# Optimization experiments

Measured on AMD Instinct MI355X. Metric: run time of the kernel, lower is better.

## Reference

```python
import jax, jax.numpy as jnp
import numpy as np

B, SV, SQ, D = 32, 4096, 1152, 128
FD = 96  # feature_dim (adaptive pool target and batchnorm channels)
BN_EPS = 1e-5


def setup_inputs() -> dict:
    key = jax.random.key(0)
    k1, k2, k3, k4 = jax.random.split(key, 4)
    return {
        'q': jax.random.normal(k1, (B, SQ, D), dtype=jnp.float32),
        'v': jax.random.normal(k2, (B, SV, D), dtype=jnp.float32),
        'h_mat': jax.random.normal(k3, (1, 3, FD, 1), dtype=jnp.float32),
        'h_bias': jax.random.normal(k4, (1, 3, 1, 1), dtype=jnp.float32),
        'gamma': jnp.ones((FD,), dtype=jnp.float32),
        'beta': jnp.zeros((FD,), dtype=jnp.float32),
    }


def reference(q, v, h_mat, h_bias, gamma, beta):
    b, sv, d = v.shape
    sq = q.shape[1]
    # einsum 'bijk,hcxk,bqiv->bjck' with a=[B,1,Sv,D], h_mat=[1,3,FD,1], b=[B,1,D,Sq]
    # (k broadcasts 1->D, i broadcasts 1->D) factorizes into independent sums:
    sumq = jnp.sum(q, axis=(1, 2))                 # [B] = sum_{i,v} b[b,0,i,v]
    hm = jnp.sum(h_mat, axis=(0, 2, 3))            # [3] = sum_{h,x} h_mat
    # att_maps (post transpose(1,2)): [B,3,Sv,D]
    att = (v[:, None, :, :] * hm[None, :, None, None] * sumq[:, None, None, None]
           + h_bias.reshape(1, 3, 1, 1))
    att = att / jnp.linalg.norm(att, axis=2, keepdims=True)  # L2 norm over Sv
    att = jax.nn.softmax(att, axis=2)                        # softmax over Sv

    # logits = einsum('bikj,bhi,bqvk->bivq', a1, att[:,:,0,:], b1)  -> [B,D,Sq,1]
    att0sum = att[:, :, 0, :].sum(axis=1)          # [B,D] sum over h of att_maps[:,:,0,:]
    qr = q.reshape(b, d, sq)                        # faithful to torch .view memory reshape
    vs = v.sum(axis=1)                              # [B,D] = sum_j a1[b,0,k,j]
    inner = jnp.einsum('bkv,bk->bv', qr, vs)        # [B,Sq]
    logits0 = att0sum[:, :, None] * inner[:, None, :]  # [B,D,Sq]
    # AdaptiveAvgPool1d(FD) on last dim (Sq multiple of FD -> reshape+mean), then transpose
    logits = logits0.reshape(b, d, FD, sq // FD).mean(axis=-1).transpose(0, 2, 1)  # [B,FD,D]

    # loop i=1..h_-1: einsum('bihc,bxv,bqkv->bi') -> per-batch scalar, pooled to [B,FD,1]
    vsum = v.sum(axis=(1, 2))                       # [B]
    qs = qr.sum(axis=2)                             # [B,D] = sum_k b1[b,0,k,v]
    for i in (1, 2):
        attisum = att[:, :, i, :].sum(axis=1)       # [B,D]
        li = vsum * jnp.sum(attisum * qs, axis=1)   # [B]
        logits = logits + li[:, None, None]         # broadcast add of [B,1,1]

    # BatchNorm1d(FD) in training mode: stats over (batch, length) per channel
    mean = logits.mean(axis=(0, 2), keepdims=True)
    var = logits.var(axis=(0, 2), keepdims=True)
    out = (logits - mean) * jax.lax.rsqrt(var + BN_EPS)
    out = out * gamma[None, :, None] + beta[None, :, None]
    return out
```

## Files before the change

kernel.cpp:

```cpp
#include <hip/hip_runtime.h>
#include <math.h>

#define BB 32
#define SV 4096
#define SQ 1152
#define DD 128
#define FD 96
#define NS 32
#define RPC (SV / NS)
#define LOG2E 1.44269504088896340f

#define OFF_G    0
#define OFF_P    393216
#define OFF_ATT0 1179648
#define OFF_LI   1183744
#define OFF_A0   1183776
#define OFF_A0S  1183808
#define OFF_IP   1183840
#define OFF_BNA  1186912
#define OFF_BNB  1187008

__global__ __launch_bounds__(256) void k_pass1(const float* __restrict__ q,
                                               const float* __restrict__ v,
                                               float* __restrict__ ws) {
    __shared__ float red[6][8][DD];
    if (blockIdx.x < 1024) {
        int b = blockIdx.x >> 5, chunk = blockIdx.x & 31;
        int lane = threadIdx.x & 31, rowg = threadIdx.x >> 5;
        int d0 = lane * 4;
        const float* base = v + ((size_t)b * SV + (size_t)chunk * RPC) * DD;
        float s1[4] = {}, s2[4] = {}, s3[4] = {}, s4[4] = {}, s5[4] = {}, s6[4] = {};
        for (int i = 0; i < RPC / 8; i++) {
            float4 x = *reinterpret_cast<const float4*>(base + (size_t)(rowg + 8 * i) * DD + d0);
            float vv[4] = {x.x, x.y, x.z, x.w};
#pragma unroll
            for (int j = 0; j < 4; j++) {
                float a = vv[j], a2 = a * a, a4 = a2 * a2;
                s1[j] += a;       s2[j] += a2;      s3[j] += a2 * a;
                s4[j] += a4;      s5[j] += a4 * a;  s6[j] += a4 * a2;
            }
        }
#pragma unroll
        for (int j = 0; j < 4; j++) {
            red[0][rowg][d0 + j] = s1[j]; red[1][rowg][d0 + j] = s2[j];
            red[2][rowg][d0 + j] = s3[j]; red[3][rowg][d0 + j] = s4[j];
            red[4][rowg][d0 + j] = s5[j]; red[5][rowg][d0 + j] = s6[j];
        }
        __syncthreads();
        for (int t = threadIdx.x; t < 6 * DD; t += 256) {
            int m = t >> 7, d = t & (DD - 1);
            float a = 0;
#pragma unroll
            for (int r = 0; r < 8; r++) a += red[m][r][d];
            ws[OFF_P + ((size_t)(b * NS + chunk) * 6 + m) * DD + d] = a;
        }
    } else {
        int g = (blockIdx.x - 1024) * 256 + threadIdx.x;
        const float4* p = reinterpret_cast<const float4*>(q + (size_t)g * 12);
        float4 a = p[0], b4 = p[1], c = p[2];
        ws[OFF_G + g] = ((a.x + a.y) + (a.z + a.w)) + ((b4.x + b4.y) + (b4.z + b4.w))
                      + ((c.x + c.y) + (c.z + c.w));
    }
}

__global__ __launch_bounds__(256) void k_finalize(const float* __restrict__ v,
                                                  const float* __restrict__ hmat,
                                                  const float* __restrict__ hbias,
                                                  float* __restrict__ ws) {
    int b = blockIdx.x, tid = threadIdx.x;
    __shared__ float Gl[DD * 97];
    __shared__ float qsl[DD], svl[DD];
    __shared__ float hm_l[3], hb_l[3];
    __shared__ float redc[10];
    __shared__ float sumq_sh;
    const float* Gb = ws + OFF_G + (size_t)b * DD * FD;
#pragma unroll
    for (int i = 0; i < 12; i++) {
        int idx = (i * 256 + tid) * 4;
        float4 x = *reinterpret_cast<const float4*>(Gb + idx);
        float xv[4] = {x.x, x.y, x.z, x.w};
#pragma unroll
        for (int j = 0; j < 4; j++) {
            int e = idx + j, dd = e / 96, f = e - dd * 96;
            Gl[dd * 97 + f] = xv[j];
        }
    }
    if (tid >= 128 && tid < 131) {
        int c = tid - 128;
        float h = 0;
        for (int x2 = 0; x2 < FD; x2++) h += hmat[c * FD + x2];
        hm_l[c] = h; hb_l[c] = hbias[c];
    }
    __syncthreads();
    float M1 = 0, M2 = 0, M3 = 0, M4 = 0, M5 = 0, M6 = 0;
    if (tid < 128) {
        const float* P = ws + OFF_P;
#pragma unroll 4
        for (int ch = 0; ch < NS; ch++) {
            const float* p = P + (size_t)(b * NS + ch) * 6 * DD + tid;
            M1 += p[0];      M2 += p[DD];     M3 += p[2 * DD];
            M4 += p[3 * DD]; M5 += p[4 * DD]; M6 += p[5 * DD];
        }
        svl[tid] = M1;
    } else {
        int d = tid - 128;
        float qs = 0;
#pragma unroll 8
        for (int f = 0; f < FD; f++) qs += Gl[d * 97 + f];
        qsl[d] = qs;
    }
    __syncthreads();
    if (tid < 64) {
        float x = qsl[tid] + qsl[tid + 64];
#pragma unroll
        for (int ofs = 32; ofs; ofs >>= 1) x += __shfl_xor(x, ofs, 64);
        if (tid == 0) sumq_sh = x;
    }
    __syncthreads();
    if (tid < 128) {
        float sumq = sumq_sh;
        float v0 = v[((size_t)b * SV + 0) * DD + tid];
        float v1 = v[((size_t)b * SV + 1) * DD + tid];
        float v2 = v[((size_t)b * SV + 2) * DD + tid];
        float att0 = 0, att1 = 0, att2 = 0;
#pragma unroll
        for (int c = 0; c < 3; c++) {
            float alpha = hm_l[c] * sumq, hb = hb_l[c];
            float n2 = alpha * alpha * M2 + 2.f * alpha * hb * M1 + (float)SV * hb * hb;
            float tt = alpha / sqrtf(n2);
            float Z = (float)SV + tt * (M1 + tt * (0.5f * M2 + tt * ((1.f / 6.f) * M3
                    + tt * ((1.f / 24.f) * M4 + tt * ((1.f / 120.f) * M5
                    + tt * (1.f / 720.f) * M6)))));
            float rz = 1.f / Z, tl = tt * LOG2E;
            att0 += exp2f(v0 * tl) * rz;
            att1 += exp2f(v1 * tl) * rz;
            att2 += exp2f(v2 * tl) * rz;
        }
        ws[OFF_ATT0 + b * DD + tid] = att0;
        float qsv = qsl[tid];
        float vals[5] = {att0, att0 * att0, att1 * qsv, att2 * qsv, M1};
#pragma unroll
        for (int i = 0; i < 5; i++) {
            float x = vals[i];
#pragma unroll
            for (int ofs = 32; ofs; ofs >>= 1) x += __shfl_xor(x, ofs, 64);
            if ((tid & 63) == 0) redc[(tid >> 6) * 5 + i] = x;
        }
    }
    __syncthreads();
    if (tid == 0) {
        float a0 = redc[0] + redc[5], a0s = redc[1] + redc[6];
        float r1 = redc[2] + redc[7], r2 = redc[3] + redc[8], vs = redc[4] + redc[9];
        ws[OFF_A0 + b] = a0; ws[OFF_A0S + b] = a0s;
        ws[OFF_LI + b] = vs * (r1 + r2);
    }
    if (tid < FD) {
        float ip = 0;
#pragma unroll 8
        for (int k = 0; k < DD; k++) ip += svl[k] * Gl[k * 97 + tid];
        ws[OFF_IP + b * FD + tid] = ip * (1.0f / 12.0f);
    }
}

__global__ void k_bnstats(const float* __restrict__ gamma, const float* __restrict__ beta,
                          float* __restrict__ ws) {
    const float* ipb = ws + OFF_IP; const float* A0b = ws + OFF_A0;
    const float* A0sb = ws + OFF_A0S; const float* lib = ws + OFF_LI;
    float* bnA = ws + OFF_BNA; float* bnB = ws + OFF_BNB;
    int f = threadIdx.x;
    if (f >= FD) return;
    double Sm = 0, Se2 = 0, Sl = 0;
#pragma unroll 4
    for (int b = 0; b < BB; b++) {
        double ip = ipb[b * FD + f], a0 = A0b[b], a0s = A0sb[b], l = lib[b];
        Sm += ip * a0;
        Se2 += ip * ip * a0s + 2.0 * ip * l * a0 + (double)DD * l * l;
        Sl += l;
    }
    double mean = Sm / ((double)BB * DD) + Sl / (double)BB;
    double var = Se2 / ((double)BB * DD) - mean * mean;
    double rstd = 1.0 / sqrt(var + 1e-5);
    float A = (float)rstd * gamma[f];
    bnA[f] = A; bnB[f] = beta[f] - (float)mean * A;
}

__global__ void k_out(const float* __restrict__ ws, float* __restrict__ out) {
    const float* att0b = ws + OFF_ATT0; const float* ipb = ws + OFF_IP;
    const float* lib = ws + OFF_LI;
    const float* bnA = ws + OFF_BNA; const float* bnB = ws + OFF_BNB;
    int idx = blockIdx.x * blockDim.x + threadIdx.x;
    int k = idx & (DD - 1);
    int bf = idx >> 7;
    int f = bf % FD;
    int b = bf / FD;
    out[idx] = (att0b[b * DD + k] * ipb[b * FD + f] + lib[b]) * bnA[f] + bnB[f];
}

extern "C" void kernel_launch(void* const* d_in, const int* in_sizes, int n_in,
                              void* d_out, int out_size, void* d_ws, size_t ws_size,
                              hipStream_t stream) {
    const float* q     = (const float*)d_in[0];
    const float* v     = (const float*)d_in[1];
    const float* hmat  = (const float*)d_in[2];
    const float* hbias = (const float*)d_in[3];
    const float* gamma = (const float*)d_in[4];
    const float* beta  = (const float*)d_in[5];
    float* out = (float*)d_out;
    float* ws = (float*)d_ws;

    k_pass1<<<2560, 256, 0, stream>>>(q, v, ws);
    k_finalize<<<BB, 256, 0, stream>>>(v, hmat, hbias, ws);
    k_bnstats<<<1, 128, 0, stream>>>(gamma, beta, ws);
    k_out<<<(BB * FD * DD) / 256, 256, 0, stream>>>(ws, out);
}
```

Measured before the change: 126.1 us.

## Fuse BN stats into output kernel, widen finalize, and cut v-reduction chunks

```diff
diff --git a/kernel.cpp b/kernel.cpp
--- a/kernel.cpp
+++ b/kernel.cpp
@@ -6,26 +6,24 @@
 #define SQ 1152
 #define DD 128
 #define FD 96
-#define NS 32
+#define NS 8
 #define RPC (SV / NS)
 #define LOG2E 1.44269504088896340f
 
 #define OFF_G    0
 #define OFF_P    393216
-#define OFF_ATT0 1179648
-#define OFF_LI   1183744
-#define OFF_A0   1183776
-#define OFF_A0S  1183808
-#define OFF_IP   1183840
-#define OFF_BNA  1186912
-#define OFF_BNB  1187008
+#define OFF_ATT0 589824
+#define OFF_LI   593920
+#define OFF_A0   593952
+#define OFF_A0S  593984
+#define OFF_IP   594016
 
 __global__ __launch_bounds__(256) void k_pass1(const float* __restrict__ q,
                                                const float* __restrict__ v,
                                                float* __restrict__ ws) {
     __shared__ float red[6][8][DD];
-    if (blockIdx.x < 1024) {
-        int b = blockIdx.x >> 5, chunk = blockIdx.x & 31;
+    if (blockIdx.x < 256) {
+        int b = blockIdx.x >> 3, chunk = blockIdx.x & 7;
         int lane = threadIdx.x & 31, rowg = threadIdx.x >> 5;
         int d0 = lane * 4;
         const float* base = v + ((size_t)b * SV + (size_t)chunk * RPC) * DD;
@@ -55,7 +53,7 @@
             ws[OFF_P + ((size_t)(b * NS + chunk) * 6 + m) * DD + d] = a;
         }
     } else {
-        int g = (blockIdx.x - 1024) * 256 + threadIdx.x;
+        int g = (blockIdx.x - 256) * 256 + threadIdx.x;
         const float4* p = reinterpret_cast<const float4*>(q + (size_t)g * 12);
         float4 a = p[0], b4 = p[1], c = p[2];
         ws[OFF_G + g] = ((a.x + a.y) + (a.z + a.w)) + ((b4.x + b4.y) + (b4.z + b4.w))
@@ -63,20 +61,28 @@
     }
 }
 
-__global__ __launch_bounds__(256) void k_finalize(const float* __restrict__ v,
-                                                  const float* __restrict__ hmat,
-                                                  const float* __restrict__ hbias,
-                                                  float* __restrict__ ws) {
+__global__ __launch_bounds__(1024) void k_finalize(const float* __restrict__ v,
+                                                   const float* __restrict__ hmat,
+                                                   const float* __restrict__ hbias,
+                                                   float* __restrict__ ws) {
     int b = blockIdx.x, tid = threadIdx.x;
     __shared__ float Gl[DD * 97];
-    __shared__ float qsl[DD], svl[DD];
+    __shared__ float Ml[6][DD];
+    __shared__ float qsl[DD];
+    __shared__ float pp[8][FD];
     __shared__ float hm_l[3], hb_l[3];
     __shared__ float redc[10];
     __shared__ float sumq_sh;
+    float v0 = 0, v1 = 0, v2 = 0;
+    if (tid < DD) {
+        v0 = v[((size_t)b * SV + 0) * DD + tid];
+        v1 = v[((size_t)b * SV + 1) * DD + tid];
+        v2 = v[((size_t)b * SV + 2) * DD + tid];
+    }
     const float* Gb = ws + OFF_G + (size_t)b * DD * FD;
 #pragma unroll
-    for (int i = 0; i < 12; i++) {
-        int idx = (i * 256 + tid) * 4;
+    for (int i = 0; i < 3; i++) {
+        int idx = (i * 1024 + tid) * 4;
         float4 x = *reinterpret_cast<const float4*>(Gb + idx);
         float xv[4] = {x.x, x.y, x.z, x.w};
 #pragma unroll
@@ -85,29 +91,29 @@
             Gl[dd * 97 + f] = xv[j];
         }
     }
-    if (tid >= 128 && tid < 131) {
-        int c = tid - 128;
-        float h = 0;
-        for (int x2 = 0; x2 < FD; x2++) h += hmat[c * FD + x2];
-        hm_l[c] = h; hb_l[c] = hbias[c];
-    }
-    __syncthreads();
-    float M1 = 0, M2 = 0, M3 = 0, M4 = 0, M5 = 0, M6 = 0;
-    if (tid < 128) {
-        const float* P = ws + OFF_P;
-#pragma unroll 4
-        for (int ch = 0; ch < NS; ch++) {
-            const float* p = P + (size_t)(b * NS + ch) * 6 * DD + tid;
-            M1 += p[0];      M2 += p[DD];     M3 += p[2 * DD];
-            M4 += p[3 * DD]; M5 += p[4 * DD]; M6 += p[5 * DD];
-        }
-        svl[tid] = M1;
-    } else {
-        int d = tid - 128;
-        float qs = 0;
-#pragma unroll 8
-        for (int f = 0; f < FD; f++) qs += Gl[d * 97 + f];
-        qsl[d] = qs;
+    if (tid < 6 * DD) {
+        int m = tid >> 7, d = tid & (DD - 1);
+        const float* p = ws + OFF_P + (size_t)b * NS * 6 * DD + m * DD + d;
+        float a = 0;
+#pragma unroll
+        for (int ch = 0; ch < NS; ch++) a += p[(size_t)ch * 6 * DD];
+        Ml[m][d] = a;
+    } else if (tid >= 768 && tid < 864) {
+        int t2 = tid - 768, c = t2 >> 5, x = t2 & 31;
+        float h = hmat[c * FD + x] + hmat[c * FD + x + 32] + hmat[c * FD + x + 64];
+        h += __shfl_xor(h, 1, 64); h += __shfl_xor(h, 2, 64);
+        h += __shfl_xor(h, 4, 64); h += __shfl_xor(h, 8, 64); h += __shfl_xor(h, 16, 64);
+        if (x == 0) { hm_l[c] = h; hb_l[c] = hbias[c]; }
+    }
+    __syncthreads();
+    {
+        int row = tid >> 3, j = tid & 7;
+        const float* gr = &Gl[row * 97 + j * 12];
+        float x = 0;
+#pragma unroll
+        for (int i = 0; i < 12; i++) x += gr[i];
+        x += __shfl_xor(x, 1, 64); x += __shfl_xor(x, 2, 64); x += __shfl_xor(x, 4, 64);
+        if (j == 0) qsl[row] = x;
     }
     __syncthreads();
     if (tid < 64) {
@@ -117,11 +123,10 @@
         if (tid == 0) sumq_sh = x;
     }
     __syncthreads();
-    if (tid < 128) {
+    if (tid < DD) {
         float sumq = sumq_sh;
-        float v0 = v[((size_t)b * SV + 0) * DD + tid];
-        float v1 = v[((size_t)b * SV + 1) * DD + tid];
-        float v2 = v[((size_t)b * SV + 2) * DD + tid];
+        float M1 = Ml[0][tid], M2 = Ml[1][tid], M3 = Ml[2][tid];
+        float M4 = Ml[3][tid], M5 = Ml[4][tid], M6 = Ml[5][tid];
         float att0 = 0, att1 = 0, att2 = 0;
 #pragma unroll
         for (int c = 0; c < 3; c++) {
@@ -148,52 +153,71 @@
         }
     }
     __syncthreads();
-    if (tid == 0) {
+    if (tid < 8 * FD) {
+        int kc = tid / FD, f = tid - kc * FD;
+        float s = 0;
+#pragma unroll
+        for (int k0 = 0; k0 < 16; k0++) {
+            int k = kc * 16 + k0;
+            s += Ml[0][k] * Gl[k * 97 + f];
+        }
+        pp[kc][f] = s;
+    } else if (tid == 1023) {
         float a0 = redc[0] + redc[5], a0s = redc[1] + redc[6];
         float r1 = redc[2] + redc[7], r2 = redc[3] + redc[8], vs = redc[4] + redc[9];
         ws[OFF_A0 + b] = a0; ws[OFF_A0S + b] = a0s;
         ws[OFF_LI + b] = vs * (r1 + r2);
     }
+    __syncthreads();
     if (tid < FD) {
-        float ip = 0;
-#pragma unroll 8
-        for (int k = 0; k < DD; k++) ip += svl[k] * Gl[k * 97 + tid];
-        ws[OFF_IP + b * FD + tid] = ip * (1.0f / 12.0f);
-    }
-}
-
-__global__ void k_bnstats(const float* __restrict__ gamma, const float* __restrict__ beta,
-                          float* __restrict__ ws) {
-    const float* ipb = ws + OFF_IP; const float* A0b = ws + OFF_A0;
-    const float* A0sb = ws + OFF_A0S; const float* lib = ws + OFF_LI;
-    float* bnA = ws + OFF_BNA; float* bnB = ws + OFF_BNB;
-    int f = threadIdx.x;
-    if (f >= FD) return;
-    double Sm = 0, Se2 = 0, Sl = 0;
+        float s = 0;
+#pragma unroll
+        for (int r = 0; r < 8; r++) s += pp[r][tid];
+        ws[OFF_IP + b * FD + tid] = s * (1.0f / 12.0f);
+    }
+}
+
+__global__ __launch_bounds__(256) void k_out(const float* __restrict__ gamma,
+                                             const float* __restrict__ beta,
+                                             const float* __restrict__ ws,
+                                             float* __restrict__ out) {
+    int b = blockIdx.x, tid = threadIdx.x;
+    __shared__ float att0l[DD], ipl[FD], bnAl[FD], bnBl[FD];
+    __shared__ float li_sh;
+    if (tid < DD) att0l[tid] = ws[OFF_ATT0 + b * DD + tid];
+    else if (tid < DD + FD) ipl[tid - DD] = ws[OFF_IP + b * FD + (tid - DD)];
+    if (tid == DD + FD) li_sh = ws[OFF_LI + b];
+    if (tid < FD) {
+        const float* ipb = ws + OFF_IP; const float* A0b = ws + OFF_A0;
+        const float* A0sb = ws + OFF_A0S; const float* lib = ws + OFF_LI;
+        double Sm = 0, Se2 = 0, Sl = 0;
 #pragma unroll 4
-    for (int b = 0; b < BB; b++) {
-        double ip = ipb[b * FD + f], a0 = A0b[b], a0s = A0sb[b], l = lib[b];
-        Sm += ip * a0;
-        Se2 += ip * ip * a0s + 2.0 * ip * l * a0 + (double)DD * l * l;
-        Sl += l;
-    }
-    double mean = Sm / ((double)BB * DD) + Sl / (double)BB;
-    double var = Se2 / ((double)BB * DD) - mean * mean;
-    double rstd = 1.0 / sqrt(var + 1e-5);
-    float A = (float)rstd * gamma[f];
-    bnA[f] = A; bnB[f] = beta[f] - (float)mean * A;
-}
-
-__global__ void k_out(const float* __restrict__ ws, float* __restrict__ out) {
-    const float* att0b = ws + OFF_ATT0; const float* ipb = ws + OFF_IP;
-    const float* lib = ws + OFF_LI;
-    const float* bnA = ws + OFF_BNA; const float* bnB = ws + OFF_BNB;
-    int idx = blockIdx.x * blockDim.x + threadIdx.x;
-    int k = idx & (DD - 1);
-    int bf = idx >> 7;
-    int f = bf % FD;
-    int b = bf / FD;
-    out[idx] = (att0b[b * DD + k] * ipb[b * FD + f] + lib[b]) * bnA[f] + bnB[f];
+        for (int bb = 0; bb < BB; bb++) {
+            double ip = ipb[bb * FD + tid], a0 = A0b[bb], a0s = A0sb[bb], l = lib[bb];
+            Sm += ip * a0;
+            Se2 += ip * ip * a0s + 2.0 * ip * l * a0 + (double)DD * l * l;
+            Sl += l;
+        }
+        double mean = Sm / ((double)BB * DD) + Sl / (double)BB;
+        double var = Se2 / ((double)BB * DD) - mean * mean;
+        double rstd = 1.0 / sqrt(var + 1e-5);
+        float A = (float)rstd * gamma[tid];
+        bnAl[tid] = A; bnBl[tid] = beta[tid] - (float)mean * A;
+    }
+    __syncthreads();
+    float li = li_sh;
+#pragma unroll
+    for (int i = 0; i < 12; i++) {
+        int o = (i * 256 + tid) * 4;
+        int f = o >> 7, k = o & (DD - 1);
+        float A = bnAl[f], Bc = bnBl[f], ip = ipl[f];
+        float base = li * A + Bc, scale = ip * A;
+        float4 av = *reinterpret_cast<const float4*>(&att0l[k]);
+        float4 r;
+        r.x = av.x * scale + base; r.y = av.y * scale + base;
+        r.z = av.z * scale + base; r.w = av.w * scale + base;
+        *reinterpret_cast<float4*>(out + (size_t)b * FD * DD + o) = r;
+    }
 }
 
 extern "C" void kernel_launch(void* const* d_in, const int* in_sizes, int n_in,
@@ -208,8 +232,7 @@
     float* out = (float*)d_out;
     float* ws = (float*)d_ws;
 
-    k_pass1<<<2560, 256, 0, stream>>>(q, v, ws);
-    k_finalize<<<BB, 256, 0, stream>>>(v, hmat, hbias, ws);
-    k_bnstats<<<1, 128, 0, stream>>>(gamma, beta, ws);
-    k_out<<<(BB * FD * DD) / 256, 256, 0, stream>>>(ws, out);
-}
+    k_pass1<<<1792, 256, 0, stream>>>(q, v, ws);
+    k_finalize<<<BB, 1024, 0, stream>>>(v, hmat, hbias, ws);
+    k_out<<<BB, 256, 0, stream>>>(gamma, beta, ws, out);
+}
```

Measured after the change: 126.3 us. Within noise of the previous version (+0.2%).
